# Kernel tuning notes

Measured on AMD Instinct MI355X. Metric: run time of the kernel, lower is better.

Reference implementation:

```python
import jax, jax.numpy as jnp
import numpy as np


def setup_inputs() -> dict:
    key = jax.random.key(0)
    k1, k2, k3, k4, k5 = jax.random.split(key, 5)
    B, A, FI = 4096, 256, 16   # batch, atoms, iso functions per atom
    Bo, FA = 512, 8            # bonds, aniso functions per bond
    return {
        "c_iso": jax.random.normal(k1, (B, A, FI), dtype=jnp.float32),
        "c_aniso": jax.random.normal(k2, (B, Bo, FA), dtype=jnp.float32),
        "int_iso": jax.random.uniform(k3, (B, A, FI), dtype=jnp.float32),
        "int_aniso": jax.random.uniform(k4, (B, Bo, FA), dtype=jnp.float32),
        "charge": jax.random.normal(k5, (B, A), dtype=jnp.float32),
    }


def reference(c_iso, c_aniso, int_iso, int_aniso, charge):
    # Bordered KKT system from the Lagrangian L(x,u) = (x-c)^T(x-c) - u (q^T x - Q):
    #   q^T x     = Q
    # Exact closed-form solution (Sherman-Morrison on the rank-1 border):
    #   u = 2 (Q - q^T c) / (q^T q),   x = c + (u/2) q
    B = c_iso.shape[0]
    c = jnp.concatenate([c_iso.reshape(B, -1), c_aniso.reshape(B, -1)], axis=1)   # [B, n]
    q = jnp.concatenate([int_iso.reshape(B, -1), int_aniso.reshape(B, -1)], axis=1)  # [B, n]
    Q = jnp.sum(charge, axis=1)                                                   # [B]
    qTc = jnp.einsum("bn,bn->b", q, c)
    qTq = jnp.einsum("bn,bn->b", q, q)
    u = 2.0 * (Q - qTc) / qTq                                                     # Lagrange multiplier [B]
    x = c + 0.5 * u[:, None] * q                                                  # [B, n]
    n_iso = c_iso.shape[1] * c_iso.shape[2]
    sol_iso = x[:, :n_iso].reshape(c_iso.shape)
    sol_aniso = x[:, n_iso:].reshape(c_aniso.shape)
    return (sol_iso, sol_aniso)
```

## Files before the change

kernel.cpp:

```cpp
#include <hip/hip_runtime.h>


#define HALF_N 4096
#define BLOCK  256

typedef float v4f __attribute__((ext_vector_type(4)));

#define KEEP(x) asm volatile("" : "+v"(x))
#define KEEP4(v) do { KEEP((v).x); KEEP((v).y); KEEP((v).z); KEEP((v).w); } while (0)

__global__ __launch_bounds__(BLOCK, 2) void qp_charge_norm_kernel(
    const float* __restrict__ c_iso,
    const float* __restrict__ c_aniso,
    const float* __restrict__ q_iso,
    const float* __restrict__ q_aniso,
    const float* __restrict__ charge,
    float* __restrict__ out,
    int B)
{
    const int b   = blockIdx.x;
    const int tid = threadIdx.x;

    const v4f* ci = (const v4f*)(c_iso   + (size_t)b * HALF_N);
    const v4f* ca = (const v4f*)(c_aniso + (size_t)b * HALF_N);
    const v4f* qi = (const v4f*)(q_iso   + (size_t)b * HALF_N);
    const v4f* qa = (const v4f*)(q_aniso + (size_t)b * HALF_N);

    v4f cv[8], qv[8];
#pragma unroll
    for (int j = 0; j < 4; ++j) {
        cv[j]     = ci[j * BLOCK + tid];
        qv[j]     = qi[j * BLOCK + tid];
        cv[j + 4] = ca[j * BLOCK + tid];
        qv[j + 4] = qa[j * BLOCK + tid];
    }
    float Qp = charge[(size_t)b * 256 + tid];
#pragma unroll
    for (int j = 0; j < 8; ++j) { KEEP4(cv[j]); KEEP4(qv[j]); }

    float qc = 0.0f, qq = 0.0f;
#pragma unroll
    for (int j = 0; j < 8; ++j) {
        qc += qv[j].x * cv[j].x + qv[j].y * cv[j].y
            + qv[j].z * cv[j].z + qv[j].w * cv[j].w;
        qq += qv[j].x * qv[j].x + qv[j].y * qv[j].y
            + qv[j].z * qv[j].z + qv[j].w * qv[j].w;
    }

#pragma unroll
    for (int off = 32; off > 0; off >>= 1) {
        qc += __shfl_down(qc, off, 64);
        qq += __shfl_down(qq, off, 64);
        Qp += __shfl_down(Qp, off, 64);
    }

    __shared__ float s_qc[4], s_qq[4], s_Q[4];
    const int wave = tid >> 6;
    if ((tid & 63) == 0) { s_qc[wave] = qc; s_qq[wave] = qq; s_Q[wave] = Qp; }
    __syncthreads();
    const float tqc = s_qc[0] + s_qc[1] + s_qc[2] + s_qc[3];
    const float tqq = s_qq[0] + s_qq[1] + s_qq[2] + s_qq[3];
    const float tQ  = s_Q[0]  + s_Q[1]  + s_Q[2]  + s_Q[3];
    const float h   = (tQ - tqc) / tqq;

    v4f* oi = (v4f*)(out + (size_t)b * HALF_N);
    v4f* oa = (v4f*)(out + (size_t)B * HALF_N + (size_t)b * HALF_N);
#pragma unroll
    for (int j = 0; j < 4; ++j) {
        v4f r = cv[j] + h * qv[j];
        __builtin_nontemporal_store(r, &oi[j * BLOCK + tid]);
        v4f s = cv[j + 4] + h * qv[j + 4];
        __builtin_nontemporal_store(s, &oa[j * BLOCK + tid]);
    }
}

extern "C" void kernel_launch(void* const* d_in, const int* in_sizes, int n_in,
                              void* d_out, int out_size, void* d_ws, size_t ws_size,
                              hipStream_t stream) {
    const float* c_iso   = (const float*)d_in[0];
    const float* c_aniso = (const float*)d_in[1];
    const float* q_iso   = (const float*)d_in[2];
    const float* q_aniso = (const float*)d_in[3];
    const float* charge  = (const float*)d_in[4];
    float* out = (float*)d_out;

    const int B = in_sizes[0] / HALF_N;

    qp_charge_norm_kernel<<<B, BLOCK, 0, stream>>>(
        c_iso, c_aniso, q_iso, q_aniso, charge, out, B);
}
```

Before: 326.6 us.

## Assign one batch row per wavefront and re-read inputs instead of holding them in registers

Each wavefront now handles a whole batch row, so the block-level shared-memory reduction and __syncthreads are replaced by a wave-local shuffle reduction. The inputs are no longer kept in registers between the reduction and the output pass. They are re-loaded from memory for the final update, which lets occupancy rise (launch bounds 4). The cost is a second read of c and q (64 KB per row), which is expected to hit L2/MALL, plus longer serial loops per wave.

Result: slower. 372.0 us (+13.9%).

```diff
diff --git a/kernel.cpp b/kernel.cpp
--- a/kernel.cpp
+++ b/kernel.cpp
@@ -3,13 +3,11 @@
 
 #define HALF_N 4096
 #define BLOCK  256
+#define WPB    4
 
 typedef float v4f __attribute__((ext_vector_type(4)));
 
-#define KEEP(x) asm volatile("" : "+v"(x))
-#define KEEP4(v) do { KEEP((v).x); KEEP((v).y); KEEP((v).z); KEEP((v).w); } while (0)
-
-__global__ __launch_bounds__(BLOCK, 2) void qp_charge_norm_kernel(
+__global__ __launch_bounds__(BLOCK, 4) void qp_charge_norm_kernel(
     const float* __restrict__ c_iso,
     const float* __restrict__ c_aniso,
     const float* __restrict__ q_iso,
@@ -18,34 +16,29 @@
     float* __restrict__ out,
     int B)
 {
-    const int b   = blockIdx.x;
-    const int tid = threadIdx.x;
+    const int tid  = threadIdx.x;
+    const int lane = tid & 63;
+    const int wave = tid >> 6;
+    const int b    = blockIdx.x * WPB + wave;
 
     const v4f* ci = (const v4f*)(c_iso   + (size_t)b * HALF_N);
     const v4f* ca = (const v4f*)(c_aniso + (size_t)b * HALF_N);
     const v4f* qi = (const v4f*)(q_iso   + (size_t)b * HALF_N);
     const v4f* qa = (const v4f*)(q_aniso + (size_t)b * HALF_N);
 
-    v4f cv[8], qv[8];
-#pragma unroll
-    for (int j = 0; j < 4; ++j) {
-        cv[j]     = ci[j * BLOCK + tid];
-        qv[j]     = qi[j * BLOCK + tid];
-        cv[j + 4] = ca[j * BLOCK + tid];
-        qv[j + 4] = qa[j * BLOCK + tid];
-    }
-    float Qp = charge[(size_t)b * 256 + tid];
-#pragma unroll
-    for (int j = 0; j < 8; ++j) { KEEP4(cv[j]); KEEP4(qv[j]); }
-
     float qc = 0.0f, qq = 0.0f;
 #pragma unroll
-    for (int j = 0; j < 8; ++j) {
-        qc += qv[j].x * cv[j].x + qv[j].y * cv[j].y
-            + qv[j].z * cv[j].z + qv[j].w * cv[j].w;
-        qq += qv[j].x * qv[j].x + qv[j].y * qv[j].y
-            + qv[j].z * qv[j].z + qv[j].w * qv[j].w;
+    for (int j = 0; j < 16; ++j) {
+        const int idx = j * 64 + lane;
+        v4f cvi = ci[idx], qvi = qi[idx];
+        v4f cva = ca[idx], qva = qa[idx];
+        qc += qvi.x * cvi.x + qvi.y * cvi.y + qvi.z * cvi.z + qvi.w * cvi.w;
+        qq += qvi.x * qvi.x + qvi.y * qvi.y + qvi.z * qvi.z + qvi.w * qvi.w;
+        qc += qva.x * cva.x + qva.y * cva.y + qva.z * cva.z + qva.w * cva.w;
+        qq += qva.x * qva.x + qva.y * qva.y + qva.z * qva.z + qva.w * qva.w;
     }
+    v4f chv = ((const v4f*)(charge + (size_t)b * 256))[lane];
+    float Qp = chv.x + chv.y + chv.z + chv.w;
 
 #pragma unroll
     for (int off = 32; off > 0; off >>= 1) {
@@ -53,24 +46,17 @@
         qq += __shfl_down(qq, off, 64);
         Qp += __shfl_down(Qp, off, 64);
     }
-
-    __shared__ float s_qc[4], s_qq[4], s_Q[4];
-    const int wave = tid >> 6;
-    if ((tid & 63) == 0) { s_qc[wave] = qc; s_qq[wave] = qq; s_Q[wave] = Qp; }
-    __syncthreads();
-    const float tqc = s_qc[0] + s_qc[1] + s_qc[2] + s_qc[3];
-    const float tqq = s_qq[0] + s_qq[1] + s_qq[2] + s_qq[3];
-    const float tQ  = s_Q[0]  + s_Q[1]  + s_Q[2]  + s_Q[3];
-    const float h   = (tQ - tqc) / tqq;
+    const float h = __shfl((Qp - qc) / qq, 0, 64);
 
     v4f* oi = (v4f*)(out + (size_t)b * HALF_N);
     v4f* oa = (v4f*)(out + (size_t)B * HALF_N + (size_t)b * HALF_N);
 #pragma unroll
-    for (int j = 0; j < 4; ++j) {
-        v4f r = cv[j] + h * qv[j];
-        __builtin_nontemporal_store(r, &oi[j * BLOCK + tid]);
-        v4f s = cv[j + 4] + h * qv[j + 4];
-        __builtin_nontemporal_store(s, &oa[j * BLOCK + tid]);
+    for (int j = 0; j < 16; ++j) {
+        const int idx = j * 64 + lane;
+        v4f r = ci[idx] + h * qi[idx];
+        __builtin_nontemporal_store(r, &oi[idx]);
+        v4f s = ca[idx] + h * qa[idx];
+        __builtin_nontemporal_store(s, &oa[idx]);
     }
 }
 
@@ -86,6 +72,6 @@
 
     const int B = in_sizes[0] / HALF_N;
 
-    qp_charge_norm_kernel<<<B, BLOCK, 0, stream>>>(
+    qp_charge_norm_kernel<<<B / WPB, BLOCK, 0, stream>>>(
         c_iso, c_aniso, q_iso, q_aniso, charge, out, B);
 }
```
